# Performance work log

Measured on AMD Instinct MI355X. Metric: run time of the kernel, lower is better.

Reference implementation:

```python
import jax, jax.numpy as jnp
import numpy as np

N, E = 50000, 600000
D_IN, D_H, D_OUT = 512, 128, 1
BN_EPS = 1e-5


def setup_inputs() -> dict:
    key = jax.random.key(0)
    ks = jax.random.split(key, 16)
    s = 0.05
    inp = {
        "feature": jax.random.normal(ks[0], (N, D_IN), dtype=jnp.float32),
        "edge_index": jax.random.randint(ks[1], (2, E), 0, N, dtype=jnp.int32),
        "head_W": jax.random.normal(ks[2], (D_IN, D_H), dtype=jnp.float32) * s,
        "head_b": jnp.zeros((D_H,), dtype=jnp.float32),
        "gin_W1": jax.random.normal(ks[3], (D_H, D_H), dtype=jnp.float32) * s,
        "gin_b1": jnp.zeros((D_H,), dtype=jnp.float32),
        "lin_W1": jax.random.normal(ks[4], (D_H, D_H), dtype=jnp.float32) * s,
        "lin_b1": jnp.zeros((D_H,), dtype=jnp.float32),
        "gin_W2": jax.random.normal(ks[5], (D_H, D_H), dtype=jnp.float32) * s,
        "gin_b2": jnp.zeros((D_H,), dtype=jnp.float32),
        "lin_W2": jax.random.normal(ks[6], (D_H, D_H), dtype=jnp.float32) * s,
        "lin_b2": jnp.zeros((D_H,), dtype=jnp.float32),
        "tail_W": jax.random.normal(ks[7], (D_H, D_OUT), dtype=jnp.float32) * s,
        "tail_b": jnp.zeros((D_OUT,), dtype=jnp.float32),
        "bn_gamma": jnp.ones((D_OUT,), dtype=jnp.float32),
        "bn_beta": jnp.zeros((D_OUT,), dtype=jnp.float32),
    }
    return inp


def _gin_layer(x, src, dst, gin_W, gin_b, lin_W, lin_b):
    # PyG GINConv, eps=0: nn((1+eps)*x + sum_{j in N(i)} x_j)
    agg = jax.ops.segment_sum(x[src], dst, num_segments=N)  # [N, D_H]
    h = jax.nn.relu((x + agg) @ gin_W + gin_b)              # GIN MLP (dropout p=0)
    return h @ lin_W + lin_b                                # plain post-linear


def reference(feature, edge_index, head_W, head_b,
              gin_W1, gin_b1, lin_W1, lin_b1,
              gin_W2, gin_b2, lin_W2, lin_b2,
              tail_W, tail_b, bn_gamma, bn_beta):
    src, dst = edge_index[0], edge_index[1]
    x = jax.nn.relu(feature @ head_W + head_b)              # head block (dropout p=0)
    x = _gin_layer(x, src, dst, gin_W1, gin_b1, lin_W1, lin_b1)
    x = _gin_layer(x, src, dst, gin_W2, gin_b2, lin_W2, lin_b2)
    z = x @ tail_W + tail_b                                 # [N, 1]
    # BatchNorm1d in training mode: biased batch stats over the node dim
    mu = jnp.mean(z, axis=0, keepdims=True)
    var = jnp.mean((z - mu) ** 2, axis=0, keepdims=True)
    return (z - mu) * jax.lax.rsqrt(var + BN_EPS) * bn_gamma + bn_beta
```

## Files before the change

kernel.cpp:

```cpp
#include <hip/hip_runtime.h>

#define N_NODES 50000
#define N_EDGES 600000
#define DH 128
#define BN_EPS 1e-5f
#define SCAN_BLOCKS ((N_NODES + 255) / 256)
#define HEAD_GRID ((N_NODES + 63) / 64)

typedef __attribute__((ext_vector_type(8))) short bf16x8;
typedef __attribute__((ext_vector_type(4))) float f32x4;

__device__ inline unsigned short f2bf(float x) {
  unsigned u = __float_as_uint(x);
  return (unsigned short)((u + 0x7FFFu + ((u >> 16) & 1u)) >> 16);
}
__device__ inline float bf2f(unsigned short h) {
  return __uint_as_float(((unsigned)h) << 16);
}

__device__ inline void gl_lds16(const unsigned short* g, unsigned short* l) {
  __builtin_amdgcn_global_load_lds(
      (const __attribute__((address_space(1))) unsigned int*)g,
      (__attribute__((address_space(3))) unsigned int*)l, 16, 0, 0);
}

__global__ __launch_bounds__(256) void convert_W5_count(
    const float* __restrict__ hW, const float* __restrict__ g1,
    const float* __restrict__ l1, const float* __restrict__ g2,
    const float* __restrict__ l2,
    unsigned short* __restrict__ hH, unsigned short* __restrict__ hL,
    unsigned short* __restrict__ g1H, unsigned short* __restrict__ g1L,
    unsigned short* __restrict__ l1H, unsigned short* __restrict__ l1L,
    unsigned short* __restrict__ g2H, unsigned short* __restrict__ g2L,
    unsigned short* __restrict__ l2H, unsigned short* __restrict__ l2L,
    const int* __restrict__ eidx, int* __restrict__ cnt) {
  int b = blockIdx.x;
  if (b >= 512) {
    int e = (b - 512) * 256 + threadIdx.x;
    if (e < N_EDGES) atomicAdd(&cnt[eidx[N_EDGES + e]], 1);
    return;
  }
  const float* W;
  unsigned short *hi, *lo;
  int idx;
  if (b < 256) {
    W = hW; hi = hH; lo = hL;
    idx = b * 256 + threadIdx.x;
  } else {
    int w = (b - 256) >> 6;
    idx = ((b - 256) & 63) * 256 + threadIdx.x;
    W = (w == 0) ? g1 : (w == 1) ? l1 : (w == 2) ? g2 : l2;
    hi = (w == 0) ? g1H : (w == 1) ? l1H : (w == 2) ? g2H : l2H;
    lo = (w == 0) ? g1L : (w == 1) ? l1L : (w == 2) ? g2L : l2L;
  }
  int k = idx >> 7;
  int n = idx & 127;
  float x = W[idx];
  unsigned short h = f2bf(x);
  unsigned short l = f2bf(x - bf2f(h));
  int kstep = k >> 5;
  int ctile = ((n >> 6) << 2) | (n & 3);
  int cs = (n >> 2) & 15;
  int lane = ((k >> 3) & 3) * 16 + cs;
  int j = k & 7;
  size_t off = ((size_t)(kstep * 8 + ctile) * 64 + lane) * 8 + j;
  hi[off] = h;
  lo[off] = l;
}

__global__ __launch_bounds__(256) void gemm_head_fill(
    const float* __restrict__ A,
    const unsigned short* __restrict__ Bh, const unsigned short* __restrict__ Bl,
    const float* __restrict__ bias, float* __restrict__ C,
    unsigned short* __restrict__ xb_out, int M,
    const int* __restrict__ eidx, const int* __restrict__ rs,
    int* __restrict__ cursor, int* __restrict__ esrc) {
  constexpr int K = 512;
  constexpr int KSTEPS = K / 64;
  constexpr int ASTR = 72;
  __shared__ __align__(16) unsigned short Ah[64 * ASTR];
  __shared__ __align__(16) unsigned short Bhs[2][4096];
  __shared__ __align__(16) unsigned short Bls[2][4096];

  if (blockIdx.x >= HEAD_GRID) {
    int e = (blockIdx.x - HEAD_GRID) * 256 + threadIdx.x;
    if (e < N_EDGES) {
      int d = eidx[N_EDGES + e];
      int p = atomicAdd(&cursor[d], 1);
      esrc[rs[d] + p] = eidx[e];
    }
    return;
  }

  const int tid = threadIdx.x;
  const int wave = tid >> 6;
  const int lane = tid & 63;
  const int m0 = blockIdx.x * 64;

  const int s_row = tid >> 2;
  const int s_grp = tid & 3;
  const int g_row = m0 + s_row;
  const int g_rowc = (g_row < M) ? g_row : (M - 1);
  const float* af = A + (size_t)g_rowc * K + s_grp * 16;

  const int rgrp = wave & 1;
  const int ch = wave >> 1;

  f32x4 acc[2][4];
#pragma unroll
  for (int r = 0; r < 2; ++r)
#pragma unroll
    for (int c = 0; c < 4; ++c) acc[r][c] = (f32x4){0.f, 0.f, 0.f, 0.f};

  for (int ks = 0; ks < KSTEPS; ++ks) {
    {
      float4 f0 = *(const float4*)(af + ks * 64);
      float4 f1 = *(const float4*)(af + ks * 64 + 4);
      float4 f2 = *(const float4*)(af + ks * 64 + 8);
      float4 f3 = *(const float4*)(af + ks * 64 + 12);
      ushort4 h0, h1, h2, h3;
      h0.x = f2bf(f0.x); h0.y = f2bf(f0.y); h0.z = f2bf(f0.z); h0.w = f2bf(f0.w);
      h1.x = f2bf(f1.x); h1.y = f2bf(f1.y); h1.z = f2bf(f1.z); h1.w = f2bf(f1.w);
      h2.x = f2bf(f2.x); h2.y = f2bf(f2.y); h2.z = f2bf(f2.z); h2.w = f2bf(f2.w);
      h3.x = f2bf(f3.x); h3.y = f2bf(f3.y); h3.z = f2bf(f3.z); h3.w = f2bf(f3.w);
      int base = s_row * ASTR + s_grp * 16;
      *(ushort4*)&Ah[base + 0] = h0;
      *(ushort4*)&Ah[base + 4] = h1;
      *(ushort4*)&Ah[base + 8] = h2;
      *(ushort4*)&Ah[base + 12] = h3;
    }
#pragma unroll
    for (int s = 0; s < 2; ++s) {
      const unsigned short* sh = Bh + (size_t)(2 * ks + s) * 4096 + wave * 1024;
      const unsigned short* sl = Bl + (size_t)(2 * ks + s) * 4096 + wave * 1024;
      gl_lds16(sh + lane * 8, &Bhs[s][wave * 1024]);
      gl_lds16(sh + 512 + lane * 8, &Bhs[s][wave * 1024 + 512]);
      gl_lds16(sl + lane * 8, &Bls[s][wave * 1024]);
      gl_lds16(sl + 512 + lane * 8, &Bls[s][wave * 1024 + 512]);
    }
    __syncthreads();

#pragma unroll
    for (int s = 0; s < 2; ++s) {
      bf16x8 a0 = *(const bf16x8*)&Ah[(rgrp * 32 + (lane & 15)) * ASTR + s * 32 + (lane >> 4) * 8];
      bf16x8 a1 = *(const bf16x8*)&Ah[(rgrp * 32 + 16 + (lane & 15)) * ASTR + s * 32 + (lane >> 4) * 8];
#pragma unroll
      for (int c = 0; c < 4; ++c) {
        int ct = ch * 4 + c;
        bf16x8 bh = *(const bf16x8*)&Bhs[s][(ct * 64 + lane) * 8];
        bf16x8 bl = *(const bf16x8*)&Bls[s][(ct * 64 + lane) * 8];
        acc[0][c] = __builtin_amdgcn_mfma_f32_16x16x32_bf16(a0, bh, acc[0][c], 0, 0, 0);
        acc[0][c] = __builtin_amdgcn_mfma_f32_16x16x32_bf16(a0, bl, acc[0][c], 0, 0, 0);
        acc[1][c] = __builtin_amdgcn_mfma_f32_16x16x32_bf16(a1, bh, acc[1][c], 0, 0, 0);
        acc[1][c] = __builtin_amdgcn_mfma_f32_16x16x32_bf16(a1, bl, acc[1][c], 0, 0, 0);
      }
    }
    __syncthreads();
  }

  const int coln = lane & 15;
  const int rown = (lane >> 4) * 4;
  const int colbase = ch * 64 + coln * 4;
  const float4 bv = *(const float4*)(bias + colbase);
#pragma unroll
  for (int r = 0; r < 2; ++r) {
#pragma unroll
    for (int reg = 0; reg < 4; ++reg) {
      int row = m0 + rgrp * 32 + r * 16 + rown + reg;
      if (row < M) {
        float4 v;
        v.x = fmaxf(acc[r][0][reg] + bv.x, 0.f);
        v.y = fmaxf(acc[r][1][reg] + bv.y, 0.f);
        v.z = fmaxf(acc[r][2][reg] + bv.z, 0.f);
        v.w = fmaxf(acc[r][3][reg] + bv.w, 0.f);
        *(float4*)&C[(size_t)row * DH + colbase] = v;
        ushort4 hb;
        hb.x = f2bf(v.x); hb.y = f2bf(v.y); hb.z = f2bf(v.z); hb.w = f2bf(v.w);
        *(ushort4*)&xb_out[(size_t)row * DH + colbase] = hb;
      }
    }
  }
}

__global__ __launch_bounds__(256) void gemm_gin(
    const unsigned short* __restrict__ yb,
    const unsigned short* __restrict__ B1h, const unsigned short* __restrict__ B1l,
    const float* __restrict__ b1,
    const unsigned short* __restrict__ B2h, const unsigned short* __restrict__ B2l,
    const float* __restrict__ b2, float* __restrict__ X,
    unsigned short* __restrict__ xb_out, int M) {
  constexpr int K = 128;
  constexpr int KSTEPS = K / 32;
  constexpr int ASTR = 40;
  constexpr int HSTR = 136;
  __shared__ __align__(16) unsigned short Ah[64 * ASTR];
  __shared__ __align__(16) unsigned short Bhs[4096];
  __shared__ __align__(16) unsigned short Bls[4096];
  __shared__ __align__(16) unsigned short Hb[64 * HSTR];

  const int tid = threadIdx.x;
  const int wave = tid >> 6;
  const int lane = tid & 63;
  const int m0 = blockIdx.x * 64;

  const int s_row = tid >> 2;
  const int s_oct = tid & 3;
  const int g_row = m0 + s_row;
  const int g_rowc = (g_row < M) ? g_row : (M - 1);
  const unsigned short* ab = yb + (size_t)g_rowc * K + s_oct * 8;

  const int rgrp = wave & 1;
  const int ch = wave >> 1;
  const int coln = lane & 15;
  const int rown = (lane >> 4) * 4;
  const int colbase = ch * 64 + coln * 4;

  auto issueB = [&](const unsigned short* Bh, const unsigned short* Bl, int ks) {
    const unsigned short* sh = Bh + (size_t)ks * 4096 + wave * 1024;
    const unsigned short* sl = Bl + (size_t)ks * 4096 + wave * 1024;
    gl_lds16(sh + lane * 8, &Bhs[wave * 1024]);
    gl_lds16(sh + 512 + lane * 8, &Bhs[wave * 1024 + 512]);
    gl_lds16(sl + lane * 8, &Bls[wave * 1024]);
    gl_lds16(sl + 512 + lane * 8, &Bls[wave * 1024 + 512]);
  };

  f32x4 acc[2][4];
#pragma unroll
  for (int r = 0; r < 2; ++r)
#pragma unroll
    for (int c = 0; c < 4; ++c) acc[r][c] = (f32x4){0.f, 0.f, 0.f, 0.f};

  for (int ks = 0; ks < KSTEPS; ++ks) {
    *(uint4*)&Ah[s_row * ASTR + s_oct * 8] = *(const uint4*)(ab + ks * 32);
    issueB(B1h, B1l, ks);
    __syncthreads();
    bf16x8 a0 = *(const bf16x8*)&Ah[(rgrp * 32 + (lane & 15)) * ASTR + (lane >> 4) * 8];
    bf16x8 a1 = *(const bf16x8*)&Ah[(rgrp * 32 + 16 + (lane & 15)) * ASTR + (lane >> 4) * 8];
#pragma unroll
    for (int c = 0; c < 4; ++c) {
      int ct = ch * 4 + c;
      bf16x8 bh = *(const bf16x8*)&Bhs[(ct * 64 + lane) * 8];
      bf16x8 bl = *(const bf16x8*)&Bls[(ct * 64 + lane) * 8];
      acc[0][c] = __builtin_amdgcn_mfma_f32_16x16x32_bf16(a0, bh, acc[0][c], 0, 0, 0);
      acc[0][c] = __builtin_amdgcn_mfma_f32_16x16x32_bf16(a0, bl, acc[0][c], 0, 0, 0);
      acc[1][c] = __builtin_amdgcn_mfma_f32_16x16x32_bf16(a1, bh, acc[1][c], 0, 0, 0);
      acc[1][c] = __builtin_amdgcn_mfma_f32_16x16x32_bf16(a1, bl, acc[1][c], 0, 0, 0);
    }
    __syncthreads();
  }

  {
    const float4 bv = *(const float4*)(b1 + colbase);
#pragma unroll
    for (int r = 0; r < 2; ++r) {
#pragma unroll
      for (int reg = 0; reg < 4; ++reg) {
        int lrow = rgrp * 32 + r * 16 + rown + reg;
        ushort4 hb;
        hb.x = f2bf(fmaxf(acc[r][0][reg] + bv.x, 0.f));
        hb.y = f2bf(fmaxf(acc[r][1][reg] + bv.y, 0.f));
        hb.z = f2bf(fmaxf(acc[r][2][reg] + bv.z, 0.f));
        hb.w = f2bf(fmaxf(acc[r][3][reg] + bv.w, 0.f));
        *(ushort4*)&Hb[lrow * HSTR + colbase] = hb;
      }
    }
#pragma unroll
    for (int r = 0; r < 2; ++r)
#pragma unroll
      for (int c = 0; c < 4; ++c) acc[r][c] = (f32x4){0.f, 0.f, 0.f, 0.f};
  }

  for (int ks = 0; ks < KSTEPS; ++ks) {
    issueB(B2h, B2l, ks);
    __syncthreads();
    bf16x8 a0 = *(const bf16x8*)&Hb[(rgrp * 32 + (lane & 15)) * HSTR + ks * 32 + (lane >> 4) * 8];
    bf16x8 a1 = *(const bf16x8*)&Hb[(rgrp * 32 + 16 + (lane & 15)) * HSTR + ks * 32 + (lane >> 4) * 8];
#pragma unroll
    for (int c = 0; c < 4; ++c) {
      int ct = ch * 4 + c;
      bf16x8 bh = *(const bf16x8*)&Bhs[(ct * 64 + lane) * 8];
      bf16x8 bl = *(const bf16x8*)&Bls[(ct * 64 + lane) * 8];
      acc[0][c] = __builtin_amdgcn_mfma_f32_16x16x32_bf16(a0, bh, acc[0][c], 0, 0, 0);
      acc[0][c] = __builtin_amdgcn_mfma_f32_16x16x32_bf16(a0, bl, acc[0][c], 0, 0, 0);
      acc[1][c] = __builtin_amdgcn_mfma_f32_16x16x32_bf16(a1, bh, acc[1][c], 0, 0, 0);
      acc[1][c] = __builtin_amdgcn_mfma_f32_16x16x32_bf16(a1, bl, acc[1][c], 0, 0, 0);
    }
    __syncthreads();
  }

  {
    const float4 bv = *(const float4*)(b2 + colbase);
#pragma unroll
    for (int r = 0; r < 2; ++r) {
#pragma unroll
      for (int reg = 0; reg < 4; ++reg) {
        int row = m0 + rgrp * 32 + r * 16 + rown + reg;
        if (row < M) {
          float4 v;
          v.x = acc[r][0][reg] + bv.x;
          v.y = acc[r][1][reg] + bv.y;
          v.z = acc[r][2][reg] + bv.z;
          v.w = acc[r][3][reg] + bv.w;
          *(float4*)&X[(size_t)row * DH + colbase] = v;
          if (xb_out) {
            ushort4 hb;
            hb.x = f2bf(v.x); hb.y = f2bf(v.y); hb.z = f2bf(v.z); hb.w = f2bf(v.w);
            *(ushort4*)&xb_out[(size_t)row * DH + colbase] = hb;
          }
        }
      }
    }
  }
}

__global__ __launch_bounds__(256) void scan_block(const int* __restrict__ cnt,
                                                  int* __restrict__ rs,
                                                  int* __restrict__ partials) {
  int t = threadIdx.x;
  int i = blockIdx.x * 256 + t;
  int v = (i < N_NODES) ? ((cnt[i] + 3) & ~3) : 0;
  __shared__ int s[256];
  s[t] = v;
  __syncthreads();
#pragma unroll
  for (int off = 1; off < 256; off <<= 1) {
    int add = (t >= off) ? s[t - off] : 0;
    __syncthreads();
    s[t] += add;
    __syncthreads();
  }
  if (i < N_NODES) rs[i] = s[t] - v;
  if (t == 255) partials[blockIdx.x] = s[255];
}

__global__ __launch_bounds__(256) void scan_partials(int* __restrict__ partials,
                                                     float* __restrict__ red) {
  int t = threadIdx.x;
  if (t == 0) { red[0] = 0.f; red[1] = 0.f; }
  int v = (t < SCAN_BLOCKS) ? partials[t] : 0;
  __shared__ int s[256];
  s[t] = v;
  __syncthreads();
#pragma unroll
  for (int off = 1; off < 256; off <<= 1) {
    int add = (t >= off) ? s[t - off] : 0;
    __syncthreads();
    s[t] += add;
    __syncthreads();
  }
  if (t < SCAN_BLOCKS) partials[t] = s[t] - v;
}

__global__ __launch_bounds__(256) void add_offsets(int* __restrict__ rs,
                                                   const int* __restrict__ partials,
                                                   const int* __restrict__ cnt) {
  int i = blockIdx.x * 256 + threadIdx.x;
  if (i < N_NODES) {
    int v = rs[i] + partials[blockIdx.x];
    rs[i] = v;
    if (i == N_NODES - 1) rs[N_NODES] = v + ((cnt[i] + 3) & ~3);
  }
}

__global__ __launch_bounds__(256) void pad_fill(const int* __restrict__ rs,
                                                int* __restrict__ cnt,
                                                int* __restrict__ esrc) {
  int i = blockIdx.x * 256 + threadIdx.x;
  if (i >= N_NODES) return;
  int d = cnt[i];
  cnt[i] = 0;
  int b = rs[i] + d;
  int e = rs[i + 1];
  for (int k = b; k < e; ++k) esrc[k] = N_NODES;
}

__global__ __launch_bounds__(256) void gin_aggregate_bf16(
    const unsigned short* __restrict__ xb, const float* __restrict__ x,
    const int* __restrict__ rs, const int* __restrict__ esrc,
    unsigned* __restrict__ yb) {
  int node = blockIdx.x * 4 + (threadIdx.x >> 6);
  int lane = threadIdx.x & 63;
  if (node >= N_NODES) return;
  float2 acc = ((const float2*)x)[(size_t)node * 64 + lane];
  const unsigned* xb2 = (const unsigned*)xb;
  int beg = rs[node];
  int end = rs[node + 1];
  int j = beg;
  for (; j + 8 <= end; j += 8) {
    int4 ia = *(const int4*)&esrc[j];
    int4 ib = *(const int4*)&esrc[j + 4];
    unsigned v0 = xb2[(size_t)ia.x * 64 + lane];
    unsigned v1 = xb2[(size_t)ia.y * 64 + lane];
    unsigned v2 = xb2[(size_t)ia.z * 64 + lane];
    unsigned v3 = xb2[(size_t)ia.w * 64 + lane];
    unsigned v4 = xb2[(size_t)ib.x * 64 + lane];
    unsigned v5 = xb2[(size_t)ib.y * 64 + lane];
    unsigned v6 = xb2[(size_t)ib.z * 64 + lane];
    unsigned v7 = xb2[(size_t)ib.w * 64 + lane];
    acc.x += ((__uint_as_float(v0 << 16) + __uint_as_float(v1 << 16)) +
              (__uint_as_float(v2 << 16) + __uint_as_float(v3 << 16))) +
             ((__uint_as_float(v4 << 16) + __uint_as_float(v5 << 16)) +
              (__uint_as_float(v6 << 16) + __uint_as_float(v7 << 16)));
    acc.y += ((__uint_as_float(v0 & 0xFFFF0000u) + __uint_as_float(v1 & 0xFFFF0000u)) +
              (__uint_as_float(v2 & 0xFFFF0000u) + __uint_as_float(v3 & 0xFFFF0000u))) +
             ((__uint_as_float(v4 & 0xFFFF0000u) + __uint_as_float(v5 & 0xFFFF0000u)) +
              (__uint_as_float(v6 & 0xFFFF0000u) + __uint_as_float(v7 & 0xFFFF0000u)));
  }
  if (j < end) {
    int4 ia = *(const int4*)&esrc[j];
    unsigned v0 = xb2[(size_t)ia.x * 64 + lane];
    unsigned v1 = xb2[(size_t)ia.y * 64 + lane];
    unsigned v2 = xb2[(size_t)ia.z * 64 + lane];
    unsigned v3 = xb2[(size_t)ia.w * 64 + lane];
    acc.x += (__uint_as_float(v0 << 16) + __uint_as_float(v1 << 16)) +
             (__uint_as_float(v2 << 16) + __uint_as_float(v3 << 16));
    acc.y += (__uint_as_float(v0 & 0xFFFF0000u) + __uint_as_float(v1 & 0xFFFF0000u)) +
             (__uint_as_float(v2 & 0xFFFF0000u) + __uint_as_float(v3 & 0xFFFF0000u));
  }
  yb[(size_t)node * 64 + lane] =
      (unsigned)f2bf(acc.x) | ((unsigned)f2bf(acc.y) << 16);
}

__global__ __launch_bounds__(256) void tail_bn1(const float* __restrict__ x,
                                                const float* __restrict__ tw,
                                                const float* __restrict__ tb,
                                                float* __restrict__ z,
                                                float* __restrict__ red) {
  const int lane = threadIdx.x & 31;
  const int grp = threadIdx.x >> 5;
  float4 w = *(const float4*)(tw + lane * 4);
  float accS = 0.f, accQ = 0.f;
  for (int node = blockIdx.x * 8 + grp; node < N_NODES; node += gridDim.x * 8) {
    float4 v = *(const float4*)(x + (size_t)node * DH + lane * 4);
    float p = v.x * w.x + v.y * w.y + v.z * w.z + v.w * w.w;
#pragma unroll
    for (int m = 16; m; m >>= 1) p += __shfl_xor(p, m, 32);
    if (lane == 0) {
      float zv = p + tb[0];
      z[node] = zv;
      accS += zv;
      accQ += zv * zv;
    }
  }
  __shared__ float sS[256];
  __shared__ float sQ[256];
  sS[threadIdx.x] = accS;
  sQ[threadIdx.x] = accQ;
  __syncthreads();
  for (int s = 128; s; s >>= 1) {
    if (threadIdx.x < s) {
      sS[threadIdx.x] += sS[threadIdx.x + s];
      sQ[threadIdx.x] += sQ[threadIdx.x + s];
    }
    __syncthreads();
  }
  if (threadIdx.x == 0) {
    atomicAdd(&red[0], sS[0]);
    atomicAdd(&red[1], sQ[0]);
  }
}

__global__ __launch_bounds__(256) void bn2(const float* __restrict__ z,
                                           const float* __restrict__ red,
                                           const float* __restrict__ gamma,
                                           const float* __restrict__ beta,
                                           float* __restrict__ out) {
  int i = blockIdx.x * 256 + threadIdx.x;
  if (i >= N_NODES) return;
  float mu = red[0] * (1.0f / N_NODES);
  float var = red[1] * (1.0f / N_NODES) - mu * mu;
  out[i] = (z[i] - mu) * rsqrtf(var + BN_EPS) * gamma[0] + beta[0];
}

extern "C" void kernel_launch(void* const* d_in, const int* in_sizes, int n_in,
                              void* d_out, int out_size, void* d_ws, size_t ws_size,
                              hipStream_t stream) {
  const float* feature = (const float*)d_in[0];
  const int* eidx = (const int*)d_in[1];
  const float* head_W = (const float*)d_in[2];
  const float* head_b = (const float*)d_in[3];
  const float* gin_W1 = (const float*)d_in[4];
  const float* gin_b1 = (const float*)d_in[5];
  const float* lin_W1 = (const float*)d_in[6];
  const float* lin_b1 = (const float*)d_in[7];
  const float* gin_W2 = (const float*)d_in[8];
  const float* gin_b2 = (const float*)d_in[9];
  const float* lin_W2 = (const float*)d_in[10];
  const float* lin_b2 = (const float*)d_in[11];
  const float* tail_W = (const float*)d_in[12];
  const float* tail_b = (const float*)d_in[13];
  const float* bn_gamma = (const float*)d_in[14];
  const float* bn_beta = (const float*)d_in[15];

  float* X = (float*)d_ws;
  float* z = X + (size_t)N_NODES * DH;
  float* red = z + N_NODES;
  int* row_start = (int*)(red + 2);
  int* cnt = row_start + (N_NODES + 1);
  int* partials = cnt + N_NODES;
  int* esrc = (int*)(((uintptr_t)(partials + 256) + 15) & ~(uintptr_t)15);
  unsigned short* wp =
      (unsigned short*)(((uintptr_t)(esrc + 760000) + 15) & ~(uintptr_t)15);
  unsigned short* hH = wp;
  unsigned short* hL = hH + 65536;
  unsigned short* g1H = hL + 65536;
  unsigned short* g1L = g1H + 16384;
  unsigned short* l1H = g1L + 16384;
  unsigned short* l1L = l1H + 16384;
  unsigned short* g2H = l1L + 16384;
  unsigned short* g2L = g2H + 16384;
  unsigned short* l2H = g2L + 16384;
  unsigned short* l2L = l2H + 16384;
  unsigned short* xb = l2L + 16384;
  unsigned short* yb = xb + (size_t)(N_NODES + 1) * DH;

  const int gin_grid = (N_NODES + 63) / 64;
  const int edge_grid = (N_EDGES + 255) / 256;
  const int agg_grid = (N_NODES + 3) / 4;

  hipMemsetAsync(cnt, 0, N_NODES * sizeof(int), stream);
  hipMemsetAsync(xb + (size_t)N_NODES * DH, 0, DH * sizeof(unsigned short), stream);

  convert_W5_count<<<512 + edge_grid, 256, 0, stream>>>(
      head_W, gin_W1, lin_W1, gin_W2, lin_W2, hH, hL, g1H, g1L, l1H, l1L,
      g2H, g2L, l2H, l2L, eidx, cnt);

  scan_block<<<SCAN_BLOCKS, 256, 0, stream>>>(cnt, row_start, partials);
  scan_partials<<<1, 256, 0, stream>>>(partials, red);
  add_offsets<<<SCAN_BLOCKS, 256, 0, stream>>>(row_start, partials, cnt);
  pad_fill<<<SCAN_BLOCKS, 256, 0, stream>>>(row_start, cnt, esrc);

  gemm_head_fill<<<HEAD_GRID + edge_grid, 256, 0, stream>>>(
      feature, hH, hL, head_b, X, xb, N_NODES, eidx, row_start, cnt, esrc);

  gin_aggregate_bf16<<<agg_grid, 256, 0, stream>>>(xb, X, row_start, esrc,
                                                   (unsigned*)yb);
  gemm_gin<<<gin_grid, 256, 0, stream>>>(yb, g1H, g1L, gin_b1, l1H, l1L,
                                         lin_b1, X, xb, N_NODES);

  gin_aggregate_bf16<<<agg_grid, 256, 0, stream>>>(xb, X, row_start, esrc,
                                                   (unsigned*)yb);
  gemm_gin<<<gin_grid, 256, 0, stream>>>(yb, g2H, g2L, gin_b2, l2H, l2L,
                                         lin_b2, X, nullptr, N_NODES);

  tail_bn1<<<512, 256, 0, stream>>>(X, tail_W, tail_b, z, red);
  bn2<<<(N_NODES + 255) / 256, 256, 0, stream>>>(z, red, bn_gamma, bn_beta, (float*)d_out);
}
```

Before: 372.6 us.

## Fuse tail projection and BN statistics into final GIN GEMM epilogue

The last gemm_gin now computes the tail dot product per row in its epilogue, using LDS partial sums across column groups, then writes z and accumulates sum and sum-of-squares with atomics. This removes the separate tail_bn1 kernel and the write and re-read of the full 50000x128 fp32 X. It also drops a memset by zeroing the padding row of xb inside the weight-conversion kernel. The cost is an extra LDS pass and more atomics, one pair per 64-row block.

```diff
diff --git a/kernel.cpp b/kernel.cpp
--- a/kernel.cpp
+++ b/kernel.cpp
@@ -33,13 +33,15 @@
     unsigned short* __restrict__ l1H, unsigned short* __restrict__ l1L,
     unsigned short* __restrict__ g2H, unsigned short* __restrict__ g2L,
     unsigned short* __restrict__ l2H, unsigned short* __restrict__ l2L,
-    const int* __restrict__ eidx, int* __restrict__ cnt) {
+    const int* __restrict__ eidx, int* __restrict__ cnt,
+    unsigned* __restrict__ xb_dummy) {
   int b = blockIdx.x;
   if (b >= 512) {
     int e = (b - 512) * 256 + threadIdx.x;
     if (e < N_EDGES) atomicAdd(&cnt[eidx[N_EDGES + e]], 1);
     return;
   }
+  if (b == 0 && threadIdx.x < 64) xb_dummy[threadIdx.x] = 0u;
   const float* W;
   unsigned short *hi, *lo;
   int idx;
@@ -188,7 +190,9 @@
     const float* __restrict__ b1,
     const unsigned short* __restrict__ B2h, const unsigned short* __restrict__ B2l,
     const float* __restrict__ b2, float* __restrict__ X,
-    unsigned short* __restrict__ xb_out, int M) {
+    unsigned short* __restrict__ xb_out, int M,
+    const float* __restrict__ tw, const float* __restrict__ tb,
+    float* __restrict__ z, float* __restrict__ red) {
   constexpr int K = 128;
   constexpr int KSTEPS = K / 32;
   constexpr int ASTR = 40;
@@ -288,8 +292,9 @@
     __syncthreads();
   }
 
-  {
-    const float4 bv = *(const float4*)(b2 + colbase);
+  const float4 bv = *(const float4*)(b2 + colbase);
+
+  if (tw == nullptr) {
 #pragma unroll
     for (int r = 0; r < 2; ++r) {
 #pragma unroll
@@ -302,12 +307,48 @@
           v.z = acc[r][2][reg] + bv.z;
           v.w = acc[r][3][reg] + bv.w;
           *(float4*)&X[(size_t)row * DH + colbase] = v;
-          if (xb_out) {
-            ushort4 hb;
-            hb.x = f2bf(v.x); hb.y = f2bf(v.y); hb.z = f2bf(v.z); hb.w = f2bf(v.w);
-            *(ushort4*)&xb_out[(size_t)row * DH + colbase] = hb;
-          }
+          ushort4 hb;
+          hb.x = f2bf(v.x); hb.y = f2bf(v.y); hb.z = f2bf(v.z); hb.w = f2bf(v.w);
+          *(ushort4*)&xb_out[(size_t)row * DH + colbase] = hb;
         }
+      }
+    }
+  } else {
+    float* zpart = (float*)Hb;
+    const float4 tw4 = *(const float4*)(tw + colbase);
+#pragma unroll
+    for (int r = 0; r < 2; ++r) {
+#pragma unroll
+      for (int reg = 0; reg < 4; ++reg) {
+        int lrow = rgrp * 32 + r * 16 + rown + reg;
+        float4 v;
+        v.x = acc[r][0][reg] + bv.x;
+        v.y = acc[r][1][reg] + bv.y;
+        v.z = acc[r][2][reg] + bv.z;
+        v.w = acc[r][3][reg] + bv.w;
+        zpart[lrow * 33 + ch * 16 + coln] =
+            v.x * tw4.x + v.y * tw4.y + v.z * tw4.z + v.w * tw4.w;
+      }
+    }
+    __syncthreads();
+    if (tid < 64) {
+      int row = m0 + tid;
+      float s = 0.f;
+#pragma unroll
+      for (int k = 0; k < 32; ++k) s += zpart[tid * 33 + k];
+      float zv = s + tb[0];
+      bool valid = row < M;
+      if (valid) z[row] = zv;
+      float a = valid ? zv : 0.f;
+      float q = valid ? zv * zv : 0.f;
+#pragma unroll
+      for (int m = 32; m; m >>= 1) {
+        a += __shfl_xor(a, m);
+        q += __shfl_xor(q, m);
+      }
+      if (tid == 0) {
+        atomicAdd(&red[0], a);
+        atomicAdd(&red[1], q);
       }
     }
   }
@@ -421,45 +462,6 @@
       (unsigned)f2bf(acc.x) | ((unsigned)f2bf(acc.y) << 16);
 }
 
-__global__ __launch_bounds__(256) void tail_bn1(const float* __restrict__ x,
-                                                const float* __restrict__ tw,
-                                                const float* __restrict__ tb,
-                                                float* __restrict__ z,
-                                                float* __restrict__ red) {
-  const int lane = threadIdx.x & 31;
-  const int grp = threadIdx.x >> 5;
-  float4 w = *(const float4*)(tw + lane * 4);
-  float accS = 0.f, accQ = 0.f;
-  for (int node = blockIdx.x * 8 + grp; node < N_NODES; node += gridDim.x * 8) {
-    float4 v = *(const float4*)(x + (size_t)node * DH + lane * 4);
-    float p = v.x * w.x + v.y * w.y + v.z * w.z + v.w * w.w;
-#pragma unroll
-    for (int m = 16; m; m >>= 1) p += __shfl_xor(p, m, 32);
-    if (lane == 0) {
-      float zv = p + tb[0];
-      z[node] = zv;
-      accS += zv;
-      accQ += zv * zv;
-    }
-  }
-  __shared__ float sS[256];
-  __shared__ float sQ[256];
-  sS[threadIdx.x] = accS;
-  sQ[threadIdx.x] = accQ;
-  __syncthreads();
-  for (int s = 128; s; s >>= 1) {
-    if (threadIdx.x < s) {
-      sS[threadIdx.x] += sS[threadIdx.x + s];
-      sQ[threadIdx.x] += sQ[threadIdx.x + s];
-    }
-    __syncthreads();
-  }
-  if (threadIdx.x == 0) {
-    atomicAdd(&red[0], sS[0]);
-    atomicAdd(&red[1], sQ[0]);
-  }
-}
-
 __global__ __launch_bounds__(256) void bn2(const float* __restrict__ z,
                                            const float* __restrict__ red,
                                            const float* __restrict__ gamma,
@@ -519,11 +521,11 @@
   const int agg_grid = (N_NODES + 3) / 4;
 
   hipMemsetAsync(cnt, 0, N_NODES * sizeof(int), stream);
-  hipMemsetAsync(xb + (size_t)N_NODES * DH, 0, DH * sizeof(unsigned short), stream);
 
   convert_W5_count<<<512 + edge_grid, 256, 0, stream>>>(
       head_W, gin_W1, lin_W1, gin_W2, lin_W2, hH, hL, g1H, g1L, l1H, l1L,
-      g2H, g2L, l2H, l2L, eidx, cnt);
+      g2H, g2L, l2H, l2L, eidx, cnt,
+      (unsigned*)(xb + (size_t)N_NODES * DH));
 
   scan_block<<<SCAN_BLOCKS, 256, 0, stream>>>(cnt, row_start, partials);
   scan_partials<<<1, 256, 0, stream>>>(partials, red);
@@ -536,13 +538,14 @@
   gin_aggregate_bf16<<<agg_grid, 256, 0, stream>>>(xb, X, row_start, esrc,
                                                    (unsigned*)yb);
   gemm_gin<<<gin_grid, 256, 0, stream>>>(yb, g1H, g1L, gin_b1, l1H, l1L,
-                                         lin_b1, X, xb, N_NODES);
+                                         lin_b1, X, xb, N_NODES,
+                                         nullptr, nullptr, nullptr, nullptr);
 
   gin_aggregate_bf16<<<agg_grid, 256, 0, stream>>>(xb, X, row_start, esrc,
                                                    (unsigned*)yb);
   gemm_gin<<<gin_grid, 256, 0, stream>>>(yb, g2H, g2L, gin_b2, l2H, l2L,
-                                         lin_b2, X, nullptr, N_NODES);
-
-  tail_bn1<<<512, 256, 0, stream>>>(X, tail_W, tail_b, z, red);
+                                         lin_b2, X, nullptr, N_NODES,
+                                         tail_W, tail_b, z, red);
+
   bn2<<<(N_NODES + 255) / 256, 256, 0, stream>>>(z, red, bn_gamma, bn_beta, (float*)d_out);
 }
```

After: 366.7 us. No clear change (-1.6%).
